# Optimization experiments

Hardware: AMD Instinct MI355X
Metric: run time of the kernel (lower is better)

Reference implementation:

```python
import jax, jax.numpy as jnp
import numpy as np
import math

DIM = 512
HEADS = 8
DHEAD = DIM // HEADS            # 64
NB_FEATURES = int(DHEAD * math.log(DHEAD))  # 266
B, N = 2, 2048
CHUNK = 128                     # chunk size for the causal scan
EPS = 1e-4


def gaussian_orthogonal_random_matrix(nb_rows, nb_cols, rng):
    # blocks of orthogonal rows (Q^T of QR of a gaussian), scaled by chi-distributed norms
    blocks = []
    n_full = nb_rows // nb_cols
    for _ in range(n_full):
        q, _ = np.linalg.qr(rng.standard_normal((nb_cols, nb_cols)))
        blocks.append(q.T)
    rem = nb_rows - n_full * nb_cols
    if rem > 0:
        q, _ = np.linalg.qr(rng.standard_normal((nb_cols, nb_cols)))
        blocks.append(q.T[:rem])
    mat = np.concatenate(blocks, axis=0)
    multiplier = np.linalg.norm(rng.standard_normal((nb_rows, nb_cols)), axis=1)
    return (multiplier[:, None] * mat).astype(np.float32)


def setup_inputs() -> dict:
    key = jax.random.key(0)
    k1, k2, k3 = jax.random.split(key, 3)
    rng = np.random.default_rng(0)
    x = jax.random.normal(k1, (B, N, DIM), dtype=jnp.float32)
    w_qkv = jax.random.normal(k2, (DIM, 3 * DIM), dtype=jnp.float32) / math.sqrt(DIM)
    w_out = jax.random.normal(k3, (DIM, DIM), dtype=jnp.float32) / math.sqrt(DIM)
    b_out = jnp.zeros((DIM,), dtype=jnp.float32)
    proj = jnp.asarray(gaussian_orthogonal_random_matrix(NB_FEATURES, DHEAD, rng))
    return {"x": x, "w_qkv": w_qkv, "w_out": w_out, "b_out": b_out, "proj": proj}


def softmax_kernel(data, proj, is_query):
    # data: [b,h,n,d], proj: [m,d]
    d = data.shape[-1]
    data_normalizer = d ** -0.25
    ratio = proj.shape[0] ** -0.5
    data_dash = jnp.einsum('bhnd,md->bhnm', data_normalizer * data, proj)
    diag_data = jnp.sum(data * data, axis=-1, keepdims=True) * 0.5 * (data_normalizer ** 2)
    if is_query:
        stab = jnp.max(data_dash, axis=-1, keepdims=True)
    else:
        stab = jnp.max(data_dash)
    return ratio * (jnp.exp(data_dash - diag_data - stab) + EPS)


def causal_linear_attention(q, k, v, chunk=CHUNK):
    # q,k: [b,h,n,m]; v: [b,h,n,d]
    # out_n = sum_m q_nm * (sum_{i<=n} k_im v_i) / (sum_{i<=n} k_im)   (per-feature normalization,
    # identical to causal_linear_attention_noncuda), computed in chunks for memory efficiency.
    b, h, n, m = q.shape
    d = v.shape[-1]
    nc = n // chunk
    qc = jnp.moveaxis(q.reshape(b, h, nc, chunk, m), 2, 0)  # [nc,b,h,C,m]
    kc = jnp.moveaxis(k.reshape(b, h, nc, chunk, m), 2, 0)
    vc = jnp.moveaxis(v.reshape(b, h, nc, chunk, d), 2, 0)

    def step(carry, inp):
        kv_state, ksum_state = carry            # [b,h,m,d], [b,h,m]
        qch, kch, vch = inp                     # [b,h,C,m], [b,h,C,m], [b,h,C,d]
        ksum = ksum_state[:, :, None, :] + jnp.cumsum(kch, axis=2)          # [b,h,C,m]
        ctx = kv_state[:, :, None, :, :] + jnp.cumsum(
            jnp.einsum('bhcm,bhcd->bhcmd', kch, vch), axis=2)               # [b,h,C,m,d]
        out = jnp.einsum('bhcm,bhcmd->bhcd', qch, ctx / ksum[..., None])
        return (ctx[:, :, -1], ksum[:, :, -1]), out

    init = (jnp.zeros((b, h, m, d), q.dtype), jnp.zeros((b, h, m), q.dtype))
    _, outs = jax.lax.scan(step, init, (qc, kc, vc))
    return jnp.moveaxis(outs, 0, 2).reshape(b, h, n, d)


def reference(x, w_qkv, w_out, b_out, proj):
    b, n, _ = x.shape
    qkv = x @ w_qkv                                   # [b,n,3*dim]
    q, k, v = jnp.split(qkv, 3, axis=-1)
    split = lambda t: t.reshape(b, n, HEADS, DHEAD).transpose(0, 2, 1, 3)  # b h n d
    q, k, v = split(q), split(k), split(v)
    qp = softmax_kernel(q, proj, is_query=True)       # [b,h,n,m]
    kp = softmax_kernel(k, proj, is_query=False)
    out = causal_linear_attention(qp, kp, v)          # [b,h,n,d]
    out = out.transpose(0, 2, 1, 3).reshape(b, n, DIM)
    return out @ w_out + b_out
```

## Files before the change

kernel.cpp:

```cpp
#include <hip/hip_runtime.h>
#include <math.h>

#define DIMX 512
#define NHEADS 8
#define DH 64
#define MF 266
#define MP 272
#define MPS 288
#define NB 2
#define NSEQ 2048
#define NROWS (NB*NSEQ)
#define NBH 16
#define CHK 64
#define NCH 32
#define EPSF 1e-4f
#define LDT 40
#define LDP 72
#define LDO 296

typedef __attribute__((ext_vector_type(8))) short short8;
typedef __attribute__((ext_vector_type(4))) float f32x4;
typedef unsigned short ushort_t;

__device__ __forceinline__ unsigned fkey(float f){
    unsigned u = __float_as_uint(f);
    return (f < 0.0f) ? ~u : (u | 0x80000000u);
}
__device__ __forceinline__ float fdec(unsigned k){
    unsigned u = (k & 0x80000000u) ? (k & 0x7fffffffu) : ~k;
    return __uint_as_float(u);
}
__device__ __forceinline__ float b2f(ushort_t u){
    return __uint_as_float(((unsigned)u) << 16);
}

__device__ __forceinline__ void bsplit(float a, ushort_t& h, ushort_t& l){
    unsigned u = __float_as_uint(a);
    unsigned r = (u + 0x7fffu + ((u >> 16) & 1u)) & 0xffff0000u;
    h = (ushort_t)(r >> 16);
    float res = a - __uint_as_float(r);
    unsigned v = __float_as_uint(res);
    unsigned r2 = v + 0x7fffu + ((v >> 16) & 1u);
    l = (ushort_t)(r2 >> 16);
}

__global__ __launch_bounds__(256) void split_kernel(
    const float* __restrict__ A, ushort_t* __restrict__ H, ushort_t* __restrict__ L, int total4)
{
    int i = blockIdx.x * 256 + threadIdx.x;
    if (i >= total4) return;
    float4 f = ((const float4*)A)[i];
    ushort_t h0,h1,h2,h3,l0,l1,l2,l3;
    bsplit(f.x,h0,l0); bsplit(f.y,h1,l1); bsplit(f.z,h2,l2); bsplit(f.w,h3,l3);
    ((ushort4*)H)[i] = make_ushort4(h0,h1,h2,h3);
    ((ushort4*)L)[i] = make_ushort4(l0,l1,l2,l3);
}

__global__ __launch_bounds__(256) void splitT_kernel(
    const float* __restrict__ W, ushort_t* __restrict__ Th, ushort_t* __restrict__ Tl,
    int K, int N)
{
    __shared__ ushort_t Sh[64][72], Sl[64][72];
    const int k0 = blockIdx.y * 64, n0 = blockIdx.x * 64;
    const int tid = threadIdx.x;
    {
        const int kk = tid >> 4, nq = (tid & 15) * 4;
        for (int p = 0; p < 4; p++) {
            int k = p*16 + kk;
            float4 f = *(const float4*)&W[(size_t)(k0 + k)*N + n0 + nq];
            ushort_t h, l;
            bsplit(f.x,h,l); Sh[nq+0][k]=h; Sl[nq+0][k]=l;
            bsplit(f.y,h,l); Sh[nq+1][k]=h; Sl[nq+1][k]=l;
            bsplit(f.z,h,l); Sh[nq+2][k]=h; Sl[nq+2][k]=l;
            bsplit(f.w,h,l); Sh[nq+3][k]=h; Sl[nq+3][k]=l;
        }
    }
    __syncthreads();
    {
        const int n = tid >> 2, ks = (tid & 3) * 16;
        for (int q = 0; q < 2; q++) {
            uint4 vh = *(const uint4*)&Sh[n][ks + q*8];
            uint4 vl = *(const uint4*)&Sl[n][ks + q*8];
            *(uint4*)&Th[(size_t)(n0 + n)*K + k0 + ks + q*8] = vh;
            *(uint4*)&Tl[(size_t)(n0 + n)*K + k0 + ks + q*8] = vl;
        }
    }
}

__global__ __launch_bounds__(256) void splitP_kernel(
    const float* __restrict__ proj, ushort_t* __restrict__ ph, ushort_t* __restrict__ pl,
    unsigned* __restrict__ gmax, float nrm)
{
    int idx = blockIdx.x * 256 + threadIdx.x;
    if (idx == 0) *gmax = 0u;
    if (idx >= MPS*64/4) return;
    int m = idx >> 4, kq = (idx & 15) * 4;
    ushort4 h4 = make_ushort4(0,0,0,0), l4 = make_ushort4(0,0,0,0);
    if (m < MF) {
        float4 f = *(const float4*)&proj[m*64 + kq];
        ushort_t hh[4], ll[4];
        bsplit(f.x*nrm,hh[0],ll[0]); bsplit(f.y*nrm,hh[1],ll[1]);
        bsplit(f.z*nrm,hh[2],ll[2]); bsplit(f.w*nrm,hh[3],ll[3]);
        h4 = make_ushort4(hh[0],hh[1],hh[2],hh[3]);
        l4 = make_ushort4(ll[0],ll[1],ll[2],ll[3]);
    }
    *(ushort4*)&ph[(size_t)m*64 + kq] = h4;
    *(ushort4*)&pl[(size_t)m*64 + kq] = l4;
}

__global__ __launch_bounds__(256) void gemm_bf16s(
    const ushort_t* __restrict__ Ah, const ushort_t* __restrict__ Al,
    const ushort_t* __restrict__ Bh, const ushort_t* __restrict__ Bl,
    const float* __restrict__ bias, float* __restrict__ C,
    int M, int N, int K)
{
    __shared__ ushort_t sAh[128*LDT], sAl[128*LDT], sBh[128*LDT], sBl[128*LDT];
    const int tid = threadIdx.x;
    const int m0 = blockIdx.y * 128, n0 = blockIdx.x * 128;
    const int lane = tid & 63, w = tid >> 6;
    const int wr = w >> 1, wc = w & 1;
    const int lr = lane & 15;
    const int lsu = (lane >> 4) * 8;
    const int r = tid >> 1, sg = (tid & 1) * 16;
    const size_t gA = (size_t)(m0 + r)*K + sg;
    const size_t gB = (size_t)(n0 + r)*K + sg;

    f32x4 acc[4][4];
    #pragma unroll
    for (int i=0;i<4;i++)
        #pragma unroll
        for (int j=0;j<4;j++) acc[i][j] = (f32x4){0.f,0.f,0.f,0.f};

    for (int k0 = 0; k0 < K; k0 += 32) {
        uint4 a0 = *(const uint4*)&Ah[gA + k0];
        uint4 a1 = *(const uint4*)&Ah[gA + k0 + 8];
        uint4 a2 = *(const uint4*)&Al[gA + k0];
        uint4 a3 = *(const uint4*)&Al[gA + k0 + 8];
        uint4 b0 = *(const uint4*)&Bh[gB + k0];
        uint4 b1 = *(const uint4*)&Bh[gB + k0 + 8];
        uint4 b2 = *(const uint4*)&Bl[gB + k0];
        uint4 b3 = *(const uint4*)&Bl[gB + k0 + 8];
        __syncthreads();
        *(uint4*)&sAh[r*LDT + sg]     = a0;
        *(uint4*)&sAh[r*LDT + sg + 8] = a1;
        *(uint4*)&sAl[r*LDT + sg]     = a2;
        *(uint4*)&sAl[r*LDT + sg + 8] = a3;
        *(uint4*)&sBh[r*LDT + sg]     = b0;
        *(uint4*)&sBh[r*LDT + sg + 8] = b1;
        *(uint4*)&sBl[r*LDT + sg]     = b2;
        *(uint4*)&sBl[r*LDT + sg + 8] = b3;
        __syncthreads();
        short8 afh[4], afl[4], bfh[4], bfl[4];
        #pragma unroll
        for (int f = 0; f < 4; f++) {
            int ra = (wr*64 + f*16 + lr)*LDT + lsu;
            int rb = (wc*64 + f*16 + lr)*LDT + lsu;
            afh[f] = *(const short8*)&sAh[ra];
            afl[f] = *(const short8*)&sAl[ra];
            bfh[f] = *(const short8*)&sBh[rb];
            bfl[f] = *(const short8*)&sBl[rb];
        }
        #pragma unroll
        for (int i = 0; i < 4; i++)
            #pragma unroll
            for (int j = 0; j < 4; j++) {
                acc[i][j] = __builtin_amdgcn_mfma_f32_16x16x32_bf16(afh[i], bfh[j], acc[i][j], 0, 0, 0);
                acc[i][j] = __builtin_amdgcn_mfma_f32_16x16x32_bf16(afh[i], bfl[j], acc[i][j], 0, 0, 0);
                acc[i][j] = __builtin_amdgcn_mfma_f32_16x16x32_bf16(afl[i], bfh[j], acc[i][j], 0, 0, 0);
            }
    }
    const int crow = (lane >> 4) * 4, ccol = lane & 15;
    #pragma unroll
    for (int i = 0; i < 4; i++) {
        #pragma unroll
        for (int j = 0; j < 4; j++) {
            int col = n0 + wc*64 + j*16 + ccol;
            float bb = bias ? bias[col] : 0.f;
            #pragma unroll
            for (int rr = 0; rr < 4; rr++) {
                int row = m0 + wr*64 + i*16 + crow + rr;
                C[(size_t)row*N + col] = acc[i][j][rr] + bb;
            }
        }
    }
}

__global__ __launch_bounds__(256) void feat_mfma3(
    const float* __restrict__ qkv,
    const ushort_t* __restrict__ pjh, const ushort_t* __restrict__ pjl,
    ushort_t* __restrict__ qph, ushort_t* __restrict__ qpl,
    ushort_t* __restrict__ kph, ushort_t* __restrict__ kpl,
    float* __restrict__ diag_out, unsigned* __restrict__ gmax, float ratio)
{
    __shared__ ushort_t outH[64*LDO];
    __shared__ ushort_t outL[64*LDO];
    __shared__ float dsqs[64];
    const int tid = threadIdx.x;
    const bool isq = (blockIdx.z == 0);
    const int coff = isq ? 0 : DIMX;
    ushort_t* __restrict__ oh = isq ? qph : kph;
    ushort_t* __restrict__ ol = isq ? qpl : kpl;
    const int bh = blockIdx.y, b = bh >> 3, h = bh & 7;
    const int n0 = blockIdx.x * 64;
    const int lane = tid & 63, w = tid >> 6;
    const int fr = lane & 15, fj = lane >> 4;

    short8 aDh[2], aDl[2];
    {
        const int row = w*16 + fr;
        const float* src = &qkv[(size_t)(b*NSEQ + n0 + row)*(3*DIMX) + coff + h*DH];
        float4 u0 = *(const float4*)&src[fj*8];
        float4 u1 = *(const float4*)&src[fj*8 + 4];
        float4 u2 = *(const float4*)&src[32 + fj*8];
        float4 u3 = *(const float4*)&src[32 + fj*8 + 4];
        float v0[8] = {u0.x,u0.y,u0.z,u0.w,u1.x,u1.y,u1.z,u1.w};
        float v1[8] = {u2.x,u2.y,u2.z,u2.w,u3.x,u3.y,u3.z,u3.w};
        float ss = 0.f;
        #pragma unroll
        for (int p = 0; p < 8; p++) ss = fmaf(v0[p],v0[p], fmaf(v1[p],v1[p], ss));
        ss += __shfl_xor(ss, 16, 64);
        ss += __shfl_xor(ss, 32, 64);
        if (fj == 0) dsqs[row] = ss;
        #pragma unroll
        for (int p = 0; p < 8; p++) {
            ushort_t hh2, ll2;
            bsplit(v0[p], hh2, ll2); aDh[0][p] = (short)hh2; aDl[0][p] = (short)ll2;
            bsplit(v1[p], hh2, ll2); aDh[1][p] = (short)hh2; aDl[1][p] = (short)ll2;
        }
    }
    const int rw = w*16 + fj*4;
    const int ccol = fr;
    float mx[4] = {-1e30f,-1e30f,-1e30f,-1e30f};

    #pragma unroll 2
    for (int mt = 0; mt < 18; ++mt) {
        const size_t rb = (size_t)(mt*16 + fr)*64 + fj*8;
        short8 b0h = *(const short8*)&pjh[rb];
        short8 b1h = *(const short8*)&pjh[rb + 32];
        short8 b0l = *(const short8*)&pjl[rb];
        short8 b1l = *(const short8*)&pjl[rb + 32];
        f32x4 acc = (f32x4){0.f,0.f,0.f,0.f};
        acc = __builtin_amdgcn_mfma_f32_16x16x32_bf16(aDh[0], b0h, acc, 0, 0, 0);
        acc = __builtin_amdgcn_mfma_f32_16x16x32_bf16(aDh[0], b0l, acc, 0, 0, 0);
        acc = __builtin_amdgcn_mfma_f32_16x16x32_bf16(aDl[0], b0h, acc, 0, 0, 0);
        acc = __builtin_amdgcn_mfma_f32_16x16x32_bf16(aDh[1], b1h, acc, 0, 0, 0);
        acc = __builtin_amdgcn_mfma_f32_16x16x32_bf16(aDh[1], b1l, acc, 0, 0, 0);
        acc = __builtin_amdgcn_mfma_f32_16x16x32_bf16(aDl[1], b1h, acc, 0, 0, 0);
        const bool validc = (mt < 16) || (mt == 16 && ccol < (MF - 256));
        #pragma unroll
        for (int rr = 0; rr < 4; rr++) {
            float v = acc[rr];
            if (validc) mx[rr] = fmaxf(mx[rr], v);
            ushort_t hh2, ll2; bsplit(v, hh2, ll2);
            outH[(rw + rr)*LDO + mt*16 + ccol] = hh2;
            outL[(rw + rr)*LDO + mt*16 + ccol] = ll2;
        }
    }

    const size_t rbase = (size_t)bh*NSEQ + n0;
    float dg0[4];
    #pragma unroll
    for (int rr = 0; rr < 4; rr++) dg0[rr] = 0.0625f * dsqs[rw + rr];

    if (isq) {
        float subv[4];
        #pragma unroll
        for (int rr = 0; rr < 4; rr++) {
            float m2 = mx[rr];
            m2 = fmaxf(m2, __shfl_xor(m2, 1, 64));
            m2 = fmaxf(m2, __shfl_xor(m2, 2, 64));
            m2 = fmaxf(m2, __shfl_xor(m2, 4, 64));
            m2 = fmaxf(m2, __shfl_xor(m2, 8, 64));
            subv[rr] = dg0[rr] + m2;
        }
        #pragma unroll 2
        for (int mt = 0; mt < 18; ++mt) {
            const bool validc = (mt < 16) || (mt == 16 && ccol < (MF - 256));
            #pragma unroll
            for (int rr = 0; rr < 4; rr++) {
                int o = (rw + rr)*LDO + mt*16 + ccol;
                float f = b2f(outH[o]) + b2f(outL[o]);
                float v = validc ? ratio*(expf(f - subv[rr]) + EPSF) : 0.f;
                ushort_t hh2, ll2; bsplit(v, hh2, ll2);
                outH[o] = hh2; outL[o] = ll2;
            }
        }
    } else {
        float wm = fmaxf(fmaxf(mx[0], mx[1]), fmaxf(mx[2], mx[3]));
        #pragma unroll
        for (int o = 1; o < 64; o <<= 1) wm = fmaxf(wm, __shfl_xor(wm, o, 64));
        if (lane == 0) atomicMax(gmax, fkey(wm));
        #pragma unroll
        for (int rr = 0; rr < 4; rr++)
            if (ccol == 0) diag_out[rbase + rw + rr] = dg0[rr];
    }
    __syncthreads();
    #pragma unroll 2
    for (int p = 0; p < 9; p++) {
        int u = tid + p*256;
        int row = u / 36, c8 = u % 36;
        *(uint4*)&oh[(rbase + row)*MPS + c8*8] = *(const uint4*)&outH[row*LDO + c8*8];
        *(uint4*)&ol[(rbase + row)*MPS + c8*8] = *(const uint4*)&outL[row*LDO + c8*8];
    }
}

__global__ __launch_bounds__(256) void kexp_kernel(
    ushort_t* __restrict__ kph, ushort_t* __restrict__ kpl,
    const float* __restrict__ diagk, const unsigned* __restrict__ gmax, float ratio)
{
    unsigned gid = blockIdx.x * 256u + threadIdx.x;
    if (gid >= (unsigned)(NBH*NSEQ*(MPS/4))) return;
    unsigned row = gid / (MPS/4);
    int mq = (int)(gid % (MPS/4)) * 4;
    const float stab = fdec(*gmax);
    const float dg = diagk[row];
    size_t idx = (size_t)row*MPS + mq;
    ushort4 h4 = *(const ushort4*)&kph[idx];
    ushort4 l4 = *(const ushort4*)&kpl[idx];
    float dv[4] = {b2f(h4.x)+b2f(l4.x), b2f(h4.y)+b2f(l4.y),
                   b2f(h4.z)+b2f(l4.z), b2f(h4.w)+b2f(l4.w)};
    ushort_t hh[4], ll[4];
    #pragma unroll
    for (int j = 0; j < 4; j++) {
        float kv = (mq + j < MF) ? ratio * (expf(dv[j] - dg - stab) + EPSF) : 0.f;
        bsplit(kv, hh[j], ll[j]);
    }
    *(ushort4*)&kph[idx] = make_ushort4(hh[0],hh[1],hh[2],hh[3]);
    *(ushort4*)&kpl[idx] = make_ushort4(ll[0],ll[1],ll[2],ll[3]);
}

__global__ __launch_bounds__(320) void chunk_sums_kernel(
    const ushort_t* __restrict__ kph, const ushort_t* __restrict__ kpl,
    const float* __restrict__ qkv,
    float* __restrict__ ckvT, float* __restrict__ cksum)
{
    __shared__ float vs[CHK][DH];
    const int tid = threadIdx.x;
    const int c = blockIdx.x, bh = blockIdx.y, b = bh >> 3, h = bh & 7;
    for (int idx = tid; idx < CHK*16; idx += 320) {
        int i = idx >> 4, q = idx & 15;
        *(float4*)&vs[i][q*4] =
            *(const float4*)&qkv[(size_t)(b*NSEQ + c*CHK + i)*(3*DIMX) + 2*DIMX + h*DH + q*4];
    }
    __syncthreads();
    if (tid >= 272) return;
    const int mg = tid % 68, dg = tid / 68;
    float acc[4][16] = {};
    float ks[4] = {0.f,0.f,0.f,0.f};
    const size_t kbase = (size_t)(bh*NSEQ + c*CHK)*MPS + mg*4;
    for (int i = 0; i < CHK; i++) {
        ushort4 kh = *(const ushort4*)&kph[kbase + (size_t)i*MPS];
        ushort4 kl = *(const ushort4*)&kpl[kbase + (size_t)i*MPS];
        float kr[4] = {b2f(kh.x)+b2f(kl.x), b2f(kh.y)+b2f(kl.y),
                       b2f(kh.z)+b2f(kl.z), b2f(kh.w)+b2f(kl.w)};
        if (dg == 0) { ks[0]+=kr[0]; ks[1]+=kr[1]; ks[2]+=kr[2]; ks[3]+=kr[3]; }
        #pragma unroll
        for (int t = 0; t < 4; t++) {
            float4 vv = *(const float4*)&vs[i][dg*16 + t*4];
            float vr[4] = {vv.x,vv.y,vv.z,vv.w};
            #pragma unroll
            for (int mi=0;mi<4;mi++){
                acc[mi][t*4+0] = fmaf(kr[mi], vr[0], acc[mi][t*4+0]);
                acc[mi][t*4+1] = fmaf(kr[mi], vr[1], acc[mi][t*4+1]);
                acc[mi][t*4+2] = fmaf(kr[mi], vr[2], acc[mi][t*4+2]);
                acc[mi][t*4+3] = fmaf(kr[mi], vr[3], acc[mi][t*4+3]);
            }
        }
    }
    const size_t tbase = (size_t)(bh*NCH + c)*64;
    #pragma unroll
    for (int dd = 0; dd < 16; dd++) {
        int d = dg*16 + dd;
        *(float4*)&ckvT[(tbase + d)*MP + mg*4] =
            make_float4(acc[0][dd], acc[1][dd], acc[2][dd], acc[3][dd]);
    }
    if (dg == 0) {
        #pragma unroll
        for (int mi=0;mi<4;mi++)
            cksum[(size_t)(bh*NCH + c)*MP + mg*4 + mi] = ks[mi];
    }
}

__global__ __launch_bounds__(256) void prefix_ckvT_kernel(
    const float* __restrict__ ckvT, ushort_t* __restrict__ cth, ushort_t* __restrict__ ctl)
{
    const int bh = blockIdx.y;
    const int dm = blockIdx.x * 256 + threadIdx.x;
    if (dm >= 64*MPS) return;
    const int d = dm / MPS, m = dm % MPS;
    if (m < MP) {
        float run = 0.f;
        #pragma unroll
        for (int c = 0; c < NCH; c++) {
            size_t row = (size_t)(bh*NCH + c)*64 + d;
            ushort_t h, l;
            bsplit(run, h, l);
            cth[row*MPS + m] = h; ctl[row*MPS + m] = l;
            run += ckvT[row*MP + m];
        }
    } else {
        #pragma unroll
        for (int c = 0; c < NCH; c++) {
            size_t row = (size_t)(bh*NCH + c)*64 + d;
            cth[row*MPS + m] = 0; ctl[row*MPS + m] = 0;
        }
    }
}

__global__ __launch_bounds__(320) void prefix_ksum_kernel(float* __restrict__ cksum)
{
    const int bh = blockIdx.x;
    const int m = threadIdx.x;
    if (m >= MP) return;
    float run = 0.f;
    #pragma unroll
    for (int c = 0; c < NCH; c++) {
        size_t idx = (size_t)(bh*NCH + c)*MP + m;
        float v = cksum[idx];
        cksum[idx] = run;
        run += v;
    }
}

__global__ __launch_bounds__(320) void qprime_kernel(
    ushort_t* __restrict__ qph, ushort_t* __restrict__ qpl,
    const ushort_t* __restrict__ kph, const ushort_t* __restrict__ kpl,
    const float* __restrict__ cksum)
{
    const int c = blockIdx.x, bh = blockIdx.y;
    const int m = threadIdx.x;
    if (m >= MPS) return;
    size_t base = (size_t)(bh*NSEQ + c*CHK)*MPS + m;
    if (m < MF) {
        float run = cksum[(size_t)(bh*NCH + c)*MP + m];
        for (int i = 0; i < CHK; i++) {
            size_t idx = base + (size_t)i*MPS;
            run += b2f(kph[idx]) + b2f(kpl[idx]);
            float q = b2f(qph[idx]) + b2f(qpl[idx]);
            q /= run;
            ushort_t h, l;
            bsplit(q, h, l);
            qph[idx] = h; qpl[idx] = l;
        }
    } else {
        for (int i = 0; i < CHK; i++) {
            size_t idx = base + (size_t)i*MPS;
            qph[idx] = 0; qpl[idx] = 0;
        }
    }
}

__global__ __launch_bounds__(256) void attn_mfma(
    const ushort_t* __restrict__ qph, const ushort_t* __restrict__ qpl,
    const ushort_t* __restrict__ kph, const ushort_t* __restrict__ kpl,
    const ushort_t* __restrict__ cth, const ushort_t* __restrict__ ctl,
    const float* __restrict__ qkv,
    ushort_t* __restrict__ aout_h, ushort_t* __restrict__ aout_l)
{
    __shared__ ushort_t tQh[64*LDT], tQl[64*LDT];
    __shared__ ushort_t tKh[64*LDT], tKl[64*LDT];
    __shared__ ushort_t tSh[64*LDT], tSl[64*LDT];
    __shared__ ushort_t VTh[64*LDP], VTl[64*LDP];
    __shared__ ushort_t Ph[64*LDP],  Pl[64*LDP];
    const int tid = threadIdx.x;
    const int c = blockIdx.x, bh = blockIdx.y, b = bh >> 3, hh = bh & 7;
    const size_t rowg = (size_t)bh*NSEQ + c*CHK;
    const size_t rowx = (size_t)b*NSEQ + c*CHK;
    const size_t sbase = (size_t)(bh*NCH + c)*64;

    {
        const int j = tid >> 2, dq = (tid & 3) * 16;
        const float* vsrc = &qkv[(rowx + j)*(3*DIMX) + 2*DIMX + hh*DH + dq];
        #pragma unroll
        for (int p = 0; p < 4; p++) {
            float4 f = *(const float4*)&vsrc[p*4];
            float vr[4] = {f.x,f.y,f.z,f.w};
            #pragma unroll
            for (int wv = 0; wv < 4; wv++) {
                ushort_t h, l;
                bsplit(vr[wv], h, l);
                VTh[(dq + p*4 + wv)*LDP + j] = h;
                VTl[(dq + p*4 + wv)*LDP + j] = l;
            }
        }
    }

    const int lane = tid & 63, w = tid >> 6;
    const int wr = w >> 1, wc = w & 1;
    const int fr = lane & 15, fk = (lane >> 4) * 8;
    const int srow = tid >> 2, sseg = (tid & 3) * 8;
    f32x4 accP[2][2], accO[2][2];
    #pragma unroll
    for (int i=0;i<2;i++)
        #pragma unroll
        for (int j=0;j<2;j++){ accP[i][j]=(f32x4){0,0,0,0}; accO[i][j]=(f32x4){0,0,0,0}; }

    for (int m0 = 0; m0 < MPS; m0 += 32) {
        uint4 gq_h = *(const uint4*)&qph[(rowg + srow)*MPS + m0 + sseg];
        uint4 gq_l = *(const uint4*)&qpl[(rowg + srow)*MPS + m0 + sseg];
        uint4 gk_h = *(const uint4*)&kph[(rowg + srow)*MPS + m0 + sseg];
        uint4 gk_l = *(const uint4*)&kpl[(rowg + srow)*MPS + m0 + sseg];
        uint4 gs_h = *(const uint4*)&cth[(sbase + srow)*MPS + m0 + sseg];
        uint4 gs_l = *(const uint4*)&ctl[(sbase + srow)*MPS + m0 + sseg];
        __syncthreads();
        *(uint4*)&tQh[srow*LDT + sseg] = gq_h;
        *(uint4*)&tQl[srow*LDT + sseg] = gq_l;
        *(uint4*)&tKh[srow*LDT + sseg] = gk_h;
        *(uint4*)&tKl[srow*LDT + sseg] = gk_l;
        *(uint4*)&tSh[srow*LDT + sseg] = gs_h;
        *(uint4*)&tSl[srow*LDT + sseg] = gs_l;
        __syncthreads();
        short8 aQh[2], aQl[2], bKh[2], bKl[2], bSh[2], bSl[2];
        #pragma unroll
        for (int f = 0; f < 2; f++) {
            int ra = (wr*32 + f*16 + fr)*LDT + fk;
            int rb = (wc*32 + f*16 + fr)*LDT + fk;
            aQh[f] = *(const short8*)&tQh[ra];
            aQl[f] = *(const short8*)&tQl[ra];
            bKh[f] = *(const short8*)&tKh[rb];
            bKl[f] = *(const short8*)&tKl[rb];
            bSh[f] = *(const short8*)&tSh[rb];
            bSl[f] = *(const short8*)&tSl[rb];
        }
        #pragma unroll
        for (int i = 0; i < 2; i++)
            #pragma unroll
            for (int j = 0; j < 2; j++) {
                accP[i][j] = __builtin_amdgcn_mfma_f32_16x16x32_bf16(aQh[i], bKh[j], accP[i][j], 0, 0, 0);
                accP[i][j] = __builtin_amdgcn_mfma_f32_16x16x32_bf16(aQh[i], bKl[j], accP[i][j], 0, 0, 0);
                accP[i][j] = __builtin_amdgcn_mfma_f32_16x16x32_bf16(aQl[i], bKh[j], accP[i][j], 0, 0, 0);
                accO[i][j] = __builtin_amdgcn_mfma_f32_16x16x32_bf16(aQh[i], bSh[j], accO[i][j], 0, 0, 0);
                accO[i][j] = __builtin_amdgcn_mfma_f32_16x16x32_bf16(aQh[i], bSl[j], accO[i][j], 0, 0, 0);
                accO[i][j] = __builtin_amdgcn_mfma_f32_16x16x32_bf16(aQl[i], bSh[j], accO[i][j], 0, 0, 0);
            }
    }

    __syncthreads();
    {
        const int crow = (lane >> 4) * 4, ccol = lane & 15;
        #pragma unroll
        for (int i = 0; i < 2; i++)
            #pragma unroll
            for (int j = 0; j < 2; j++) {
                int colg = wc*32 + j*16 + ccol;
                #pragma unroll
                for (int rr = 0; rr < 4; rr++) {
                    int rowg2 = wr*32 + i*16 + crow + rr;
                    float v = (colg <= rowg2) ? accP[i][j][rr] : 0.f;
                    ushort_t h, l;
                    bsplit(v, h, l);
                    Ph[rowg2*LDP + colg] = h;
                    Pl[rowg2*LDP + colg] = l;
                }
            }
    }
    __syncthreads();

    #pragma unroll
    for (int js = 0; js < 2; js++) {
        short8 aPh[2], aPl[2], bVh[2], bVl[2];
        #pragma unroll
        for (int f = 0; f < 2; f++) {
            int ra = (wr*32 + f*16 + fr)*LDP + js*32 + fk;
            int rb = (wc*32 + f*16 + fr)*LDP + js*32 + fk;
            aPh[f] = *(const short8*)&Ph[ra];
            aPl[f] = *(const short8*)&Pl[ra];
            bVh[f] = *(const short8*)&VTh[rb];
            bVl[f] = *(const short8*)&VTl[rb];
        }
        #pragma unroll
        for (int i = 0; i < 2; i++)
            #pragma unroll
            for (int j = 0; j < 2; j++) {
                accO[i][j] = __builtin_amdgcn_mfma_f32_16x16x32_bf16(aPh[i], bVh[j], accO[i][j], 0, 0, 0);
                accO[i][j] = __builtin_amdgcn_mfma_f32_16x16x32_bf16(aPh[i], bVl[j], accO[i][j], 0, 0, 0);
                accO[i][j] = __builtin_amdgcn_mfma_f32_16x16x32_bf16(aPl[i], bVh[j], accO[i][j], 0, 0, 0);
            }
    }

    __syncthreads();
    {
        const int crow = (lane >> 4) * 4, ccol = lane & 15;
        #pragma unroll
        for (int i = 0; i < 2; i++)
            #pragma unroll
            for (int j = 0; j < 2; j++) {
                int d = wc*32 + j*16 + ccol;
                #pragma unroll
                for (int rr = 0; rr < 4; rr++) {
                    int row = wr*32 + i*16 + crow + rr;
                    ushort_t h, l;
                    bsplit(accO[i][j][rr], h, l);
                    Ph[row*LDP + d] = h;
                    Pl[row*LDP + d] = l;
                }
            }
    }
    __syncthreads();
    #pragma unroll
    for (int p = 0; p < 2; p++) {
        int u = tid + p*256;
        int row = u >> 3, c8 = u & 7;
        size_t o = (rowx + row)*DIMX + hh*DH + c8*8;
        *(uint4*)&aout_h[o] = *(const uint4*)&Ph[row*LDP + c8*8];
        *(uint4*)&aout_l[o] = *(const uint4*)&Pl[row*LDP + c8*8];
    }
}

extern "C" void kernel_launch(void* const* d_in, const int* in_sizes, int n_in,
                              void* d_out, int out_size, void* d_ws, size_t ws_size,
                              hipStream_t stream)
{
    (void)in_sizes; (void)n_in; (void)out_size; (void)ws_size;
    const float* x     = (const float*)d_in[0];
    const float* w_qkv = (const float*)d_in[1];
    const float* w_out = (const float*)d_in[2];
    const float* b_out = (const float*)d_in[3];
    const float* proj  = (const float*)d_in[4];
    float* out = (float*)d_out;

    char* ws = (char*)d_ws;
    size_t off = 0;
    auto alloc = [&](size_t bytes) -> char* {
        char* p = ws + off;
        off += (bytes + 255) & ~(size_t)255;
        return p;
    };
    float* qkv       = (float*)alloc((size_t)NROWS*3*DIMX*sizeof(float));
    float* ckvT      = (float*)alloc((size_t)NBH*NCH*64*MP*sizeof(float));
    ushort_t* qph    = (ushort_t*)alloc((size_t)NBH*NSEQ*MPS*sizeof(ushort_t));
    ushort_t* qpl    = (ushort_t*)alloc((size_t)NBH*NSEQ*MPS*sizeof(ushort_t));
    ushort_t* kph    = (ushort_t*)alloc((size_t)NBH*NSEQ*MPS*sizeof(ushort_t));
    ushort_t* kpl    = (ushort_t*)alloc((size_t)NBH*NSEQ*MPS*sizeof(ushort_t));
    ushort_t* cth    = (ushort_t*)alloc((size_t)NBH*NCH*64*MPS*sizeof(ushort_t));
    ushort_t* ctl    = (ushort_t*)alloc((size_t)NBH*NCH*64*MPS*sizeof(ushort_t));
    float* cksum     = (float*)alloc((size_t)NBH*NCH*MP*sizeof(float));
    float* diagk     = (float*)alloc((size_t)NBH*NSEQ*sizeof(float));
    unsigned* gmax   = (unsigned*)alloc(256);
    ushort_t* xs_h   = (ushort_t*)alloc((size_t)NROWS*DIMX*sizeof(ushort_t));
    ushort_t* xs_l   = (ushort_t*)alloc((size_t)NROWS*DIMX*sizeof(ushort_t));
    ushort_t* wqt_h  = (ushort_t*)alloc((size_t)(3*DIMX)*DIMX*sizeof(ushort_t));
    ushort_t* wqt_l  = (ushort_t*)alloc((size_t)(3*DIMX)*DIMX*sizeof(ushort_t));
    ushort_t* wot_h  = (ushort_t*)alloc((size_t)DIMX*DIMX*sizeof(ushort_t));
    ushort_t* wot_l  = (ushort_t*)alloc((size_t)DIMX*DIMX*sizeof(ushort_t));
    ushort_t* pjh    = (ushort_t*)alloc((size_t)MPS*64*sizeof(ushort_t));
    ushort_t* pjl    = (ushort_t*)alloc((size_t)MPS*64*sizeof(ushort_t));
    ushort_t* aout_h = xs_h;
    ushort_t* aout_l = xs_l;

    const float nrm   = (float)pow(64.0, -0.25);
    const float ratio = (float)(1.0 / sqrt(266.0));

    split_kernel<<<dim3((NROWS*DIMX/4 + 255)/256), 256, 0, stream>>>(x, xs_h, xs_l, NROWS*DIMX/4);
    splitT_kernel<<<dim3(3*DIMX/64, DIMX/64), 256, 0, stream>>>(w_qkv, wqt_h, wqt_l, DIMX, 3*DIMX);
    splitT_kernel<<<dim3(DIMX/64, DIMX/64), 256, 0, stream>>>(w_out, wot_h, wot_l, DIMX, DIMX);
    splitP_kernel<<<dim3((MPS*64/4 + 255)/256), 256, 0, stream>>>(proj, pjh, pjl, gmax, nrm);
    gemm_bf16s<<<dim3(3*DIMX/128, NROWS/128), 256, 0, stream>>>(
        xs_h, xs_l, wqt_h, wqt_l, nullptr, qkv, NROWS, 3*DIMX, DIMX);
    feat_mfma3<<<dim3(32, 16, 2), 256, 0, stream>>>(
        qkv, pjh, pjl, qph, qpl, kph, kpl, diagk, gmax, ratio);
    kexp_kernel<<<dim3((NBH*NSEQ*(MPS/4) + 255)/256), 256, 0, stream>>>(
        kph, kpl, diagk, gmax, ratio);
    chunk_sums_kernel<<<dim3(NCH, NBH), 320, 0, stream>>>(kph, kpl, qkv, ckvT, cksum);
    prefix_ckvT_kernel<<<dim3((64*MPS + 255)/256, NBH), 256, 0, stream>>>(ckvT, cth, ctl);
    prefix_ksum_kernel<<<dim3(NBH), 320, 0, stream>>>(cksum);
    qprime_kernel<<<dim3(NCH, NBH), 320, 0, stream>>>(qph, qpl, kph, kpl, cksum);
    attn_mfma<<<dim3(NCH, NBH), 256, 0, stream>>>(
        qph, qpl, kph, kpl, cth, ctl, qkv, aout_h, aout_l);
    gemm_bf16s<<<dim3(DIMX/128, NROWS/128), 256, 0, stream>>>(
        aout_h, aout_l, wot_h, wot_l, b_out, out, NROWS, DIMX, DIMX);
}
```

Measured before the change: 255.8 us.

## Transpose feature MFMA so each lane holds a full row, drop LDS staging

The feature-map kernel now swaps the MFMA operands so projection rows are the A operand and data rows the B operand. Each lane's accumulators then cover many features of one token, and all 18 tiles stay in registers. The per-row max becomes a cross-lane shuffle over two lanes. Results are written straight to global memory as ushort4 stores instead of through a 74KB shared-memory staging buffer with a barrier. This removes the LDS traffic and the occupancy limit from the large shared array, at the cost of 72 accumulator registers per lane and narrower global stores.

After: 255.0 us. No clear change (-0.3%).

```diff
diff --git a/kernel.cpp b/kernel.cpp
--- a/kernel.cpp
+++ b/kernel.cpp
@@ -16,7 +16,6 @@
 #define EPSF 1e-4f
 #define LDT 40
 #define LDP 72
-#define LDO 296
 
 typedef __attribute__((ext_vector_type(8))) short short8;
 typedef __attribute__((ext_vector_type(4))) float f32x4;
@@ -185,16 +184,13 @@
     }
 }
 
-__global__ __launch_bounds__(256) void feat_mfma3(
+__global__ __launch_bounds__(256) void feat_mfma4(
     const float* __restrict__ qkv,
     const ushort_t* __restrict__ pjh, const ushort_t* __restrict__ pjl,
     ushort_t* __restrict__ qph, ushort_t* __restrict__ qpl,
     ushort_t* __restrict__ kph, ushort_t* __restrict__ kpl,
     float* __restrict__ diag_out, unsigned* __restrict__ gmax, float ratio)
 {
-    __shared__ ushort_t outH[64*LDO];
-    __shared__ ushort_t outL[64*LDO];
-    __shared__ float dsqs[64];
     const int tid = threadIdx.x;
     const bool isq = (blockIdx.z == 0);
     const int coff = isq ? 0 : DIMX;
@@ -203,16 +199,17 @@
     const int bh = blockIdx.y, b = bh >> 3, h = bh & 7;
     const int n0 = blockIdx.x * 64;
     const int lane = tid & 63, w = tid >> 6;
-    const int fr = lane & 15, fj = lane >> 4;
-
-    short8 aDh[2], aDl[2];
+    const int cn = lane & 15, g = lane >> 4;
+
+    short8 bDh[2], bDl[2];
+    float dg;
     {
-        const int row = w*16 + fr;
+        const int row = w*16 + cn;
         const float* src = &qkv[(size_t)(b*NSEQ + n0 + row)*(3*DIMX) + coff + h*DH];
-        float4 u0 = *(const float4*)&src[fj*8];
-        float4 u1 = *(const float4*)&src[fj*8 + 4];
-        float4 u2 = *(const float4*)&src[32 + fj*8];
-        float4 u3 = *(const float4*)&src[32 + fj*8 + 4];
+        float4 u0 = *(const float4*)&src[g*8];
+        float4 u1 = *(const float4*)&src[g*8 + 4];
+        float4 u2 = *(const float4*)&src[32 + g*8];
+        float4 u3 = *(const float4*)&src[32 + g*8 + 4];
         float v0[8] = {u0.x,u0.y,u0.z,u0.w,u1.x,u1.y,u1.z,u1.w};
         float v1[8] = {u2.x,u2.y,u2.z,u2.w,u3.x,u3.y,u3.z,u3.w};
         float ss = 0.f;
@@ -220,87 +217,78 @@
         for (int p = 0; p < 8; p++) ss = fmaf(v0[p],v0[p], fmaf(v1[p],v1[p], ss));
         ss += __shfl_xor(ss, 16, 64);
         ss += __shfl_xor(ss, 32, 64);
-        if (fj == 0) dsqs[row] = ss;
+        dg = 0.0625f * ss;
         #pragma unroll
         for (int p = 0; p < 8; p++) {
             ushort_t hh2, ll2;
-            bsplit(v0[p], hh2, ll2); aDh[0][p] = (short)hh2; aDl[0][p] = (short)ll2;
-            bsplit(v1[p], hh2, ll2); aDh[1][p] = (short)hh2; aDl[1][p] = (short)ll2;
-        }
-    }
-    const int rw = w*16 + fj*4;
-    const int ccol = fr;
-    float mx[4] = {-1e30f,-1e30f,-1e30f,-1e30f};
-
-    #pragma unroll 2
+            bsplit(v0[p], hh2, ll2); bDh[0][p] = (short)hh2; bDl[0][p] = (short)ll2;
+            bsplit(v1[p], hh2, ll2); bDh[1][p] = (short)hh2; bDl[1][p] = (short)ll2;
+        }
+    }
+    f32x4 acc[18];
+    #pragma unroll
+    for (int t = 0; t < 18; t++) acc[t] = (f32x4){0.f,0.f,0.f,0.f};
+    #pragma unroll
     for (int mt = 0; mt < 18; ++mt) {
-        const size_t rb = (size_t)(mt*16 + fr)*64 + fj*8;
-        short8 b0h = *(const short8*)&pjh[rb];
-        short8 b1h = *(const short8*)&pjh[rb + 32];
-        short8 b0l = *(const short8*)&pjl[rb];
-        short8 b1l = *(const short8*)&pjl[rb + 32];
-        f32x4 acc = (f32x4){0.f,0.f,0.f,0.f};
-        acc = __builtin_amdgcn_mfma_f32_16x16x32_bf16(aDh[0], b0h, acc, 0, 0, 0);
-        acc = __builtin_amdgcn_mfma_f32_16x16x32_bf16(aDh[0], b0l, acc, 0, 0, 0);
-        acc = __builtin_amdgcn_mfma_f32_16x16x32_bf16(aDl[0], b0h, acc, 0, 0, 0);
-        acc = __builtin_amdgcn_mfma_f32_16x16x32_bf16(aDh[1], b1h, acc, 0, 0, 0);
-        acc = __builtin_amdgcn_mfma_f32_16x16x32_bf16(aDh[1], b1l, acc, 0, 0, 0);
-        acc = __builtin_amdgcn_mfma_f32_16x16x32_bf16(aDl[1], b1h, acc, 0, 0, 0);
-        const bool validc = (mt < 16) || (mt == 16 && ccol < (MF - 256));
-        #pragma unroll
-        for (int rr = 0; rr < 4; rr++) {
-            float v = acc[rr];
-            if (validc) mx[rr] = fmaxf(mx[rr], v);
-            ushort_t hh2, ll2; bsplit(v, hh2, ll2);
-            outH[(rw + rr)*LDO + mt*16 + ccol] = hh2;
-            outL[(rw + rr)*LDO + mt*16 + ccol] = ll2;
-        }
-    }
-
-    const size_t rbase = (size_t)bh*NSEQ + n0;
-    float dg0[4];
-    #pragma unroll
-    for (int rr = 0; rr < 4; rr++) dg0[rr] = 0.0625f * dsqs[rw + rr];
+        const size_t rb = (size_t)(mt*16 + cn)*64 + g*8;
+        short8 a0h = *(const short8*)&pjh[rb];
+        short8 a1h = *(const short8*)&pjh[rb + 32];
+        short8 a0l = *(const short8*)&pjl[rb];
+        short8 a1l = *(const short8*)&pjl[rb + 32];
+        acc[mt] = __builtin_amdgcn_mfma_f32_16x16x32_bf16(a0h, bDh[0], acc[mt], 0, 0, 0);
+        acc[mt] = __builtin_amdgcn_mfma_f32_16x16x32_bf16(a0h, bDl[0], acc[mt], 0, 0, 0);
+        acc[mt] = __builtin_amdgcn_mfma_f32_16x16x32_bf16(a0l, bDh[0], acc[mt], 0, 0, 0);
+        acc[mt] = __builtin_amdgcn_mfma_f32_16x16x32_bf16(a1h, bDh[1], acc[mt], 0, 0, 0);
+        acc[mt] = __builtin_amdgcn_mfma_f32_16x16x32_bf16(a1h, bDl[1], acc[mt], 0, 0, 0);
+        acc[mt] = __builtin_amdgcn_mfma_f32_16x16x32_bf16(a1l, bDh[1], acc[mt], 0, 0, 0);
+    }
+    const size_t orow = ((size_t)bh*NSEQ + n0 + w*16 + cn)*MPS;
+    const int mbase0 = g*4;
 
     if (isq) {
-        float subv[4];
-        #pragma unroll
-        for (int rr = 0; rr < 4; rr++) {
-            float m2 = mx[rr];
-            m2 = fmaxf(m2, __shfl_xor(m2, 1, 64));
-            m2 = fmaxf(m2, __shfl_xor(m2, 2, 64));
-            m2 = fmaxf(m2, __shfl_xor(m2, 4, 64));
-            m2 = fmaxf(m2, __shfl_xor(m2, 8, 64));
-            subv[rr] = dg0[rr] + m2;
-        }
-        #pragma unroll 2
+        float mx = -1e30f;
+        #pragma unroll
         for (int mt = 0; mt < 18; ++mt) {
-            const bool validc = (mt < 16) || (mt == 16 && ccol < (MF - 256));
             #pragma unroll
             for (int rr = 0; rr < 4; rr++) {
-                int o = (rw + rr)*LDO + mt*16 + ccol;
-                float f = b2f(outH[o]) + b2f(outL[o]);
-                float v = validc ? ratio*(expf(f - subv[rr]) + EPSF) : 0.f;
-                ushort_t hh2, ll2; bsplit(v, hh2, ll2);
-                outH[o] = hh2; outL[o] = ll2;
-            }
+                int m = mt*16 + mbase0 + rr;
+                if (m < MF) mx = fmaxf(mx, acc[mt][rr]);
+            }
+        }
+        mx = fmaxf(mx, __shfl_xor(mx, 16, 64));
+        mx = fmaxf(mx, __shfl_xor(mx, 32, 64));
+        const float sub = dg + mx;
+        #pragma unroll
+        for (int mt = 0; mt < 18; ++mt) {
+            ushort_t hh[4], ll[4];
+            #pragma unroll
+            for (int rr = 0; rr < 4; rr++) {
+                int m = mt*16 + mbase0 + rr;
+                float v = (m < MF) ? ratio*(expf(acc[mt][rr] - sub) + EPSF) : 0.f;
+                bsplit(v, hh[rr], ll[rr]);
+            }
+            *(ushort4*)&oh[orow + mt*16 + mbase0] = make_ushort4(hh[0],hh[1],hh[2],hh[3]);
+            *(ushort4*)&ol[orow + mt*16 + mbase0] = make_ushort4(ll[0],ll[1],ll[2],ll[3]);
         }
     } else {
-        float wm = fmaxf(fmaxf(mx[0], mx[1]), fmaxf(mx[2], mx[3]));
+        if (g == 0) diag_out[(size_t)bh*NSEQ + n0 + w*16 + cn] = dg;
+        float wm = -1e30f;
+        #pragma unroll
+        for (int mt = 0; mt < 18; ++mt) {
+            ushort_t hh[4], ll[4];
+            #pragma unroll
+            for (int rr = 0; rr < 4; rr++) {
+                int m = mt*16 + mbase0 + rr;
+                float v = (m < MF) ? acc[mt][rr] : 0.f;
+                if (m < MF) wm = fmaxf(wm, v);
+                bsplit(v, hh[rr], ll[rr]);
+            }
+            *(ushort4*)&oh[orow + mt*16 + mbase0] = make_ushort4(hh[0],hh[1],hh[2],hh[3]);
+            *(ushort4*)&ol[orow + mt*16 + mbase0] = make_ushort4(ll[0],ll[1],ll[2],ll[3]);
+        }
         #pragma unroll
         for (int o = 1; o < 64; o <<= 1) wm = fmaxf(wm, __shfl_xor(wm, o, 64));
         if (lane == 0) atomicMax(gmax, fkey(wm));
-        #pragma unroll
-        for (int rr = 0; rr < 4; rr++)
-            if (ccol == 0) diag_out[rbase + rw + rr] = dg0[rr];
-    }
-    __syncthreads();
-    #pragma unroll 2
-    for (int p = 0; p < 9; p++) {
-        int u = tid + p*256;
-        int row = u / 36, c8 = u % 36;
-        *(uint4*)&oh[(rbase + row)*MPS + c8*8] = *(const uint4*)&outH[row*LDO + c8*8];
-        *(uint4*)&ol[(rbase + row)*MPS + c8*8] = *(const uint4*)&outL[row*LDO + c8*8];
     }
 }
 
@@ -657,7 +645,7 @@
     splitP_kernel<<<dim3((MPS*64/4 + 255)/256), 256, 0, stream>>>(proj, pjh, pjl, gmax, nrm);
     gemm_bf16s<<<dim3(3*DIMX/128, NROWS/128), 256, 0, stream>>>(
         xs_h, xs_l, wqt_h, wqt_l, nullptr, qkv, NROWS, 3*DIMX, DIMX);
-    feat_mfma3<<<dim3(32, 16, 2), 256, 0, stream>>>(
+    feat_mfma4<<<dim3(32, 16, 2), 256, 0, stream>>>(
         qkv, pjh, pjl, qph, qpl, kph, kpl, diagk, gmax, ratio);
     kexp_kernel<<<dim3((NBH*NSEQ*(MPS/4) + 255)/256), 256, 0, stream>>>(
         kph, kpl, diagk, gmax, ratio);
```
